# Performance work log

Measured on AMD Instinct MI355X. Metric: run time of the kernel, lower is better.

The kernel has to match this reference:

```python
import jax, jax.numpy as jnp
import numpy as np

B, S, D = 64, 4096, 1024

def setup_inputs() -> dict:
    key = jax.random.key(0)
    k1, k2, k3, k4, k5, k6 = jax.random.split(key, 6)
    scale = 1.0 / np.sqrt(D)
    return {
        "query": jax.random.normal(k1, (B, D), dtype=jnp.float32),
        "context": jax.random.normal(k2, (B, S, D), dtype=jnp.float32),
        "context_mask": jax.random.randint(k3, (B, S), 0, 2, dtype=jnp.int32),
        "W_align": jax.random.normal(k4, (D, D), dtype=jnp.float32) * scale,
        "W_context": jax.random.normal(k5, (D, D), dtype=jnp.float32) * scale,
        "W_query": jax.random.normal(k6, (D, D), dtype=jnp.float32) * scale,
    }

def reference(query, context, context_mask, W_align, W_context, W_query):
    # alignment_function == 'general': q = query @ W_align.T   [B, D]
    q = query @ W_align.T
    # scores: context [B,S,D] bmm q [B,D,1] -> [B,S]
    align = jnp.einsum('bsd,bd->bs', context, q)
    align = jnp.where(context_mask == 0, -jnp.inf, align)
    attention = jax.nn.softmax(align, axis=-1)              # [B, S]
    weight_context = jnp.einsum('bs,bsd->bd', attention, context)  # [B, D]
    out = jnp.tanh(weight_context @ W_context.T + query @ W_query.T)
    return out, attention, weight_context
```

## Files before the change

kernel.cpp:

```cpp
#include <hip/hip_runtime.h>
#include <cstddef>
#include <cstdint>

#define B_ 64
#define S_ 4096
#define D_ 1024
#define CHUNKS 16
#define ROWS (S_ / CHUNKS)

__global__ __launch_bounds__(256) void small_gemm(
    const float* __restrict__ A1, const float* __restrict__ W1,
    const float* __restrict__ A2, const float* __restrict__ W2,
    float* __restrict__ C, int do_tanh)
{
    int t = threadIdx.x;
    int i = blockIdx.x * 4 + (t & 3);
    int b = t >> 2;

    const float4* A14 = (const float4*)(A1 + (size_t)b * D_);
    const float4* W14 = (const float4*)(W1 + (size_t)i * D_);
    float acc = 0.f;
#pragma unroll 4
    for (int k = 0; k < D_ / 4; ++k) {
        float4 a = A14[k];
        float4 w = W14[k];
        acc += a.x * w.x + a.y * w.y + a.z * w.z + a.w * w.w;
    }
    if (A2 != nullptr) {
        const float4* A24 = (const float4*)(A2 + (size_t)b * D_);
        const float4* W24 = (const float4*)(W2 + (size_t)i * D_);
#pragma unroll 4
        for (int k = 0; k < D_ / 4; ++k) {
            float4 a = A24[k];
            float4 w = W24[k];
            acc += a.x * w.x + a.y * w.y + a.z * w.z + a.w * w.w;
        }
    }
    if (do_tanh) acc = tanhf(acc);
    C[(size_t)b * D_ + i] = acc;
}

__global__ __launch_bounds__(256) void pass1(
    const float* __restrict__ ctx,
    const int* __restrict__ mask,
    const float* __restrict__ q,
    float* __restrict__ align_out,
    float* __restrict__ pm,
    float* __restrict__ pl,
    float* __restrict__ pacc)
{
    int b = blockIdx.y, c = blockIdx.x, t = threadIdx.x;
    int wave = t >> 6, lane = t & 63;

    __shared__ float4 qs[256];
    __shared__ float red[2][4][4];

    qs[t] = ((const float4*)(q + (size_t)b * D_))[t];
    __syncthreads();
    float4 qv = qs[t];

    const float* cb = ctx + (size_t)b * S_ * D_ + (size_t)c * ROWS * D_;
    const int* mb = mask + (size_t)b * S_ + c * ROWS;
    float* ab = align_out + (size_t)b * S_ + c * ROWS;

    float m = -1e30f, l = 0.f;
    float a0 = 0.f, a1 = 0.f, a2 = 0.f, a3 = 0.f;

    for (int r0 = 0; r0 < ROWS; r0 += 4) {
        int buf = (r0 >> 2) & 1;
        float4 v0 = ((const float4*)(cb + (size_t)(r0 + 0) * D_))[t];
        float4 v1 = ((const float4*)(cb + (size_t)(r0 + 1) * D_))[t];
        float4 v2 = ((const float4*)(cb + (size_t)(r0 + 2) * D_))[t];
        float4 v3 = ((const float4*)(cb + (size_t)(r0 + 3) * D_))[t];

        float p0 = v0.x * qv.x + v0.y * qv.y + v0.z * qv.z + v0.w * qv.w;
        float p1 = v1.x * qv.x + v1.y * qv.y + v1.z * qv.z + v1.w * qv.w;
        float p2 = v2.x * qv.x + v2.y * qv.y + v2.z * qv.z + v2.w * qv.w;
        float p3 = v3.x * qv.x + v3.y * qv.y + v3.z * qv.z + v3.w * qv.w;

#pragma unroll
        for (int off = 32; off > 0; off >>= 1) {
            p0 += __shfl_down(p0, off);
            p1 += __shfl_down(p1, off);
            p2 += __shfl_down(p2, off);
            p3 += __shfl_down(p3, off);
        }
        if (lane == 0) {
            red[buf][wave][0] = p0;
            red[buf][wave][1] = p1;
            red[buf][wave][2] = p2;
            red[buf][wave][3] = p3;
        }
        __syncthreads();

        float s0 = red[buf][0][0] + red[buf][1][0] + red[buf][2][0] + red[buf][3][0];
        float s1 = red[buf][0][1] + red[buf][1][1] + red[buf][2][1] + red[buf][3][1];
        float s2 = red[buf][0][2] + red[buf][1][2] + red[buf][2][2] + red[buf][3][2];
        float s3 = red[buf][0][3] + red[buf][1][3] + red[buf][2][3] + red[buf][3][3];

        int m0 = mb[r0 + 0], m1 = mb[r0 + 1], m2 = mb[r0 + 2], m3 = mb[r0 + 3];
        s0 = m0 ? s0 : -1e30f;
        s1 = m1 ? s1 : -1e30f;
        s2 = m2 ? s2 : -1e30f;
        s3 = m3 ? s3 : -1e30f;

        if (t == 0) {
            ab[r0 + 0] = s0;
            ab[r0 + 1] = s1;
            ab[r0 + 2] = s2;
            ab[r0 + 3] = s3;
        }

        float nm = fmaxf(m, fmaxf(fmaxf(s0, s1), fmaxf(s2, s3)));
        float alpha = expf(m - nm);
        float e0 = (s0 <= -1e29f) ? 0.f : expf(s0 - nm);
        float e1 = (s1 <= -1e29f) ? 0.f : expf(s1 - nm);
        float e2 = (s2 <= -1e29f) ? 0.f : expf(s2 - nm);
        float e3 = (s3 <= -1e29f) ? 0.f : expf(s3 - nm);

        l = l * alpha + (e0 + e1 + e2 + e3);
        a0 = a0 * alpha + e0 * v0.x + e1 * v1.x + e2 * v2.x + e3 * v3.x;
        a1 = a1 * alpha + e0 * v0.y + e1 * v1.y + e2 * v2.y + e3 * v3.y;
        a2 = a2 * alpha + e0 * v0.z + e1 * v1.z + e2 * v2.z + e3 * v3.z;
        a3 = a3 * alpha + e0 * v0.w + e1 * v1.w + e2 * v2.w + e3 * v3.w;
        m = nm;
    }

    int idx = b * CHUNKS + c;
    if (t == 0) {
        pm[idx] = m;
        pl[idx] = l;
    }
    float4 av;
    av.x = a0; av.y = a1; av.z = a2; av.w = a3;
    ((float4*)(pacc + (size_t)idx * D_))[t] = av;
}

__global__ __launch_bounds__(256) void combine(
    const float* __restrict__ pm, const float* __restrict__ pl,
    const float* __restrict__ pacc,
    float* __restrict__ wc, float* __restrict__ ml)
{
    int b = blockIdx.x, t = threadIdx.x;
    float m = -1e30f;
#pragma unroll
    for (int c = 0; c < CHUNKS; ++c) m = fmaxf(m, pm[b * CHUNKS + c]);
    float l = 0.f;
    float w[CHUNKS];
#pragma unroll
    for (int c = 0; c < CHUNKS; ++c) {
        w[c] = expf(pm[b * CHUNKS + c] - m);
        l += pl[b * CHUNKS + c] * w[c];
    }
    float inv = (l > 0.f) ? 1.f / l : 0.f;
    float ax = 0.f, ay = 0.f, az = 0.f, aw = 0.f;
#pragma unroll
    for (int c = 0; c < CHUNKS; ++c) {
        float4 a = ((const float4*)(pacc + (size_t)(b * CHUNKS + c) * D_))[t];
        ax += a.x * w[c];
        ay += a.y * w[c];
        az += a.z * w[c];
        aw += a.w * w[c];
    }
    float4 r;
    r.x = ax * inv; r.y = ay * inv; r.z = az * inv; r.w = aw * inv;
    ((float4*)(wc + (size_t)b * D_))[t] = r;
    if (t == 0) {
        ml[b * 2 + 0] = m;
        ml[b * 2 + 1] = l;
    }
}

__global__ __launch_bounds__(256) void finalize_att(
    float* __restrict__ att, const float* __restrict__ ml)
{
    int idx = blockIdx.x * 256 + threadIdx.x;
    int b = idx >> 12;
    float s = att[idx];
    float m = ml[b * 2 + 0], l = ml[b * 2 + 1];
    float v = (s <= -1e29f || !(l > 0.f)) ? 0.f : expf(s - m) / l;
    att[idx] = v;
}

extern "C" void kernel_launch(void* const* d_in, const int* in_sizes, int n_in,
                              void* d_out, int out_size, void* d_ws, size_t ws_size,
                              hipStream_t stream)
{
    const float* query     = (const float*)d_in[0];
    const float* ctx       = (const float*)d_in[1];
    const int*   mask      = (const int*)d_in[2];
    const float* W_align   = (const float*)d_in[3];
    const float* W_context = (const float*)d_in[4];
    const float* W_query   = (const float*)d_in[5];

    float* out = (float*)d_out;
    float* att = out + B_ * D_;
    float* wc  = att + B_ * S_;

    float* ws    = (float*)d_ws;
    float* qproj = ws;
    float* pm    = qproj + B_ * D_;
    float* pl    = pm + B_ * CHUNKS;
    float* ml    = pl + B_ * CHUNKS;
    float* pacc  = ml + 2 * B_;

    small_gemm<<<dim3(D_ / 4), 256, 0, stream>>>(query, W_align, nullptr, nullptr, qproj, 0);

    pass1<<<dim3(CHUNKS, B_), 256, 0, stream>>>(ctx, mask, qproj, att, pm, pl, pacc);

    combine<<<dim3(B_), 256, 0, stream>>>(pm, pl, pacc, wc, ml);

    finalize_att<<<dim3(B_ * S_ / 256), 256, 0, stream>>>(att, ml);

    small_gemm<<<dim3(D_ / 4), 256, 0, stream>>>(wc, W_context, query, W_query, out, 1);
}
```

Measured before the change: 1.461 ms.

## Give each wave its own row chunk to drop block-level syncs in pass1

pass1 now assigns every wave an independent run of context rows. Each lane holds a full 1024-wide row slice as four float4 loads, so row dot products finish with a wave-level xor shuffle instead of shared-memory reduction and a __syncthreads per four rows. This quadruples the number of partial softmax chunks, so combine reads and merges 64 partials per batch instead of 16. small_gemm also gets four independent accumulators for more ILP. Register pressure in pass1 rises sharply, with 16 float4 loads plus 16 accumulators per lane, which may lower occupancy.

```diff
diff --git a/kernel.cpp b/kernel.cpp
--- a/kernel.cpp
+++ b/kernel.cpp
@@ -5,8 +5,14 @@
 #define B_ 64
 #define S_ 4096
 #define D_ 1024
-#define CHUNKS 16
-#define ROWS (S_ / CHUNKS)
+#define NBLK 16
+#define WAVES 4
+#define NCH (NBLK * WAVES)
+#define WROWS (S_ / NCH)
+
+__device__ __forceinline__ float dot4(float4 a, float4 b) {
+    return a.x * b.x + a.y * b.y + a.z * b.z + a.w * b.w;
+}
 
 __global__ __launch_bounds__(256) void small_gemm(
     const float* __restrict__ A1, const float* __restrict__ W1,
@@ -19,23 +25,34 @@
 
     const float4* A14 = (const float4*)(A1 + (size_t)b * D_);
     const float4* W14 = (const float4*)(W1 + (size_t)i * D_);
-    float acc = 0.f;
-#pragma unroll 4
-    for (int k = 0; k < D_ / 4; ++k) {
-        float4 a = A14[k];
-        float4 w = W14[k];
-        acc += a.x * w.x + a.y * w.y + a.z * w.z + a.w * w.w;
+    float acc0 = 0.f, acc1 = 0.f, acc2 = 0.f, acc3 = 0.f;
+#pragma unroll 2
+    for (int k = 0; k < D_ / 4; k += 4) {
+        float4 a0 = A14[k + 0], w0 = W14[k + 0];
+        float4 a1 = A14[k + 1], w1 = W14[k + 1];
+        float4 a2 = A14[k + 2], w2 = W14[k + 2];
+        float4 a3 = A14[k + 3], w3 = W14[k + 3];
+        acc0 += dot4(a0, w0);
+        acc1 += dot4(a1, w1);
+        acc2 += dot4(a2, w2);
+        acc3 += dot4(a3, w3);
     }
     if (A2 != nullptr) {
         const float4* A24 = (const float4*)(A2 + (size_t)b * D_);
         const float4* W24 = (const float4*)(W2 + (size_t)i * D_);
-#pragma unroll 4
-        for (int k = 0; k < D_ / 4; ++k) {
-            float4 a = A24[k];
-            float4 w = W24[k];
-            acc += a.x * w.x + a.y * w.y + a.z * w.z + a.w * w.w;
+#pragma unroll 2
+        for (int k = 0; k < D_ / 4; k += 4) {
+            float4 a0 = A24[k + 0], w0 = W24[k + 0];
+            float4 a1 = A24[k + 1], w1 = W24[k + 1];
+            float4 a2 = A24[k + 2], w2 = W24[k + 2];
+            float4 a3 = A24[k + 3], w3 = W24[k + 3];
+            acc0 += dot4(a0, w0);
+            acc1 += dot4(a1, w1);
+            acc2 += dot4(a2, w2);
+            acc3 += dot4(a3, w3);
         }
     }
+    float acc = (acc0 + acc1) + (acc2 + acc3);
     if (do_tanh) acc = tanhf(acc);
     C[(size_t)b * D_ + i] = acc;
 }
@@ -49,67 +66,57 @@
     float* __restrict__ pl,
     float* __restrict__ pacc)
 {
-    int b = blockIdx.y, c = blockIdx.x, t = threadIdx.x;
-    int wave = t >> 6, lane = t & 63;
-
-    __shared__ float4 qs[256];
-    __shared__ float red[2][4][4];
-
-    qs[t] = ((const float4*)(q + (size_t)b * D_))[t];
-    __syncthreads();
-    float4 qv = qs[t];
-
-    const float* cb = ctx + (size_t)b * S_ * D_ + (size_t)c * ROWS * D_;
-    const int* mb = mask + (size_t)b * S_ + c * ROWS;
-    float* ab = align_out + (size_t)b * S_ + c * ROWS;
+    int b = blockIdx.y;
+    int lane = threadIdx.x & 63;
+    int c = blockIdx.x * WAVES + (threadIdx.x >> 6);
+
+    const float4* qb = (const float4*)(q + (size_t)b * D_);
+    float4 q0 = qb[lane];
+    float4 q1 = qb[lane + 64];
+    float4 q2 = qb[lane + 128];
+    float4 q3 = qb[lane + 192];
+
+    const float4* cb = (const float4*)(ctx + (size_t)b * S_ * D_ + (size_t)c * WROWS * D_);
+    const int* mb = mask + (size_t)b * S_ + c * WROWS;
+    float* ab = align_out + (size_t)b * S_ + c * WROWS;
 
     float m = -1e30f, l = 0.f;
-    float a0 = 0.f, a1 = 0.f, a2 = 0.f, a3 = 0.f;
-
-    for (int r0 = 0; r0 < ROWS; r0 += 4) {
-        int buf = (r0 >> 2) & 1;
-        float4 v0 = ((const float4*)(cb + (size_t)(r0 + 0) * D_))[t];
-        float4 v1 = ((const float4*)(cb + (size_t)(r0 + 1) * D_))[t];
-        float4 v2 = ((const float4*)(cb + (size_t)(r0 + 2) * D_))[t];
-        float4 v3 = ((const float4*)(cb + (size_t)(r0 + 3) * D_))[t];
-
-        float p0 = v0.x * qv.x + v0.y * qv.y + v0.z * qv.z + v0.w * qv.w;
-        float p1 = v1.x * qv.x + v1.y * qv.y + v1.z * qv.z + v1.w * qv.w;
-        float p2 = v2.x * qv.x + v2.y * qv.y + v2.z * qv.z + v2.w * qv.w;
-        float p3 = v3.x * qv.x + v3.y * qv.y + v3.z * qv.z + v3.w * qv.w;
+    float4 a0 = make_float4(0.f, 0.f, 0.f, 0.f);
+    float4 a1 = a0, a2 = a0, a3 = a0;
+
+    for (int r0 = 0; r0 < WROWS; r0 += 4) {
+        const float4* row0 = cb + (size_t)(r0 + 0) * (D_ / 4);
+        const float4* row1 = cb + (size_t)(r0 + 1) * (D_ / 4);
+        const float4* row2 = cb + (size_t)(r0 + 2) * (D_ / 4);
+        const float4* row3 = cb + (size_t)(r0 + 3) * (D_ / 4);
+
+        float4 v00 = row0[lane], v01 = row0[lane + 64], v02 = row0[lane + 128], v03 = row0[lane + 192];
+        float4 v10 = row1[lane], v11 = row1[lane + 64], v12 = row1[lane + 128], v13 = row1[lane + 192];
+        float4 v20 = row2[lane], v21 = row2[lane + 64], v22 = row2[lane + 128], v23 = row2[lane + 192];
+        float4 v30 = row3[lane], v31 = row3[lane + 64], v32 = row3[lane + 128], v33 = row3[lane + 192];
+
+        int mk0 = mb[r0 + 0], mk1 = mb[r0 + 1], mk2 = mb[r0 + 2], mk3 = mb[r0 + 3];
+
+        float p0 = dot4(v00, q0) + dot4(v01, q1) + dot4(v02, q2) + dot4(v03, q3);
+        float p1 = dot4(v10, q0) + dot4(v11, q1) + dot4(v12, q2) + dot4(v13, q3);
+        float p2 = dot4(v20, q0) + dot4(v21, q1) + dot4(v22, q2) + dot4(v23, q3);
+        float p3 = dot4(v30, q0) + dot4(v31, q1) + dot4(v32, q2) + dot4(v33, q3);
 
 #pragma unroll
         for (int off = 32; off > 0; off >>= 1) {
-            p0 += __shfl_down(p0, off);
-            p1 += __shfl_down(p1, off);
-            p2 += __shfl_down(p2, off);
-            p3 += __shfl_down(p3, off);
+            p0 += __shfl_xor(p0, off);
+            p1 += __shfl_xor(p1, off);
+            p2 += __shfl_xor(p2, off);
+            p3 += __shfl_xor(p3, off);
         }
-        if (lane == 0) {
-            red[buf][wave][0] = p0;
-            red[buf][wave][1] = p1;
-            red[buf][wave][2] = p2;
-            red[buf][wave][3] = p3;
-        }
-        __syncthreads();
-
-        float s0 = red[buf][0][0] + red[buf][1][0] + red[buf][2][0] + red[buf][3][0];
-        float s1 = red[buf][0][1] + red[buf][1][1] + red[buf][2][1] + red[buf][3][1];
-        float s2 = red[buf][0][2] + red[buf][1][2] + red[buf][2][2] + red[buf][3][2];
-        float s3 = red[buf][0][3] + red[buf][1][3] + red[buf][2][3] + red[buf][3][3];
-
-        int m0 = mb[r0 + 0], m1 = mb[r0 + 1], m2 = mb[r0 + 2], m3 = mb[r0 + 3];
-        s0 = m0 ? s0 : -1e30f;
-        s1 = m1 ? s1 : -1e30f;
-        s2 = m2 ? s2 : -1e30f;
-        s3 = m3 ? s3 : -1e30f;
-
-        if (t == 0) {
-            ab[r0 + 0] = s0;
-            ab[r0 + 1] = s1;
-            ab[r0 + 2] = s2;
-            ab[r0 + 3] = s3;
-        }
+
+        float s0 = mk0 ? p0 : -1e30f;
+        float s1 = mk1 ? p1 : -1e30f;
+        float s2 = mk2 ? p2 : -1e30f;
+        float s3 = mk3 ? p3 : -1e30f;
+
+        float sv = (lane == 0) ? s0 : (lane == 1) ? s1 : (lane == 2) ? s2 : s3;
+        if (lane < 4) ab[r0 + lane] = sv;
 
         float nm = fmaxf(m, fmaxf(fmaxf(s0, s1), fmaxf(s2, s3)));
         float alpha = expf(m - nm);
@@ -119,21 +126,40 @@
         float e3 = (s3 <= -1e29f) ? 0.f : expf(s3 - nm);
 
         l = l * alpha + (e0 + e1 + e2 + e3);
-        a0 = a0 * alpha + e0 * v0.x + e1 * v1.x + e2 * v2.x + e3 * v3.x;
-        a1 = a1 * alpha + e0 * v0.y + e1 * v1.y + e2 * v2.y + e3 * v3.y;
-        a2 = a2 * alpha + e0 * v0.z + e1 * v1.z + e2 * v2.z + e3 * v3.z;
-        a3 = a3 * alpha + e0 * v0.w + e1 * v1.w + e2 * v2.w + e3 * v3.w;
+
+        a0.x = a0.x * alpha + e0 * v00.x + e1 * v10.x + e2 * v20.x + e3 * v30.x;
+        a0.y = a0.y * alpha + e0 * v00.y + e1 * v10.y + e2 * v20.y + e3 * v30.y;
+        a0.z = a0.z * alpha + e0 * v00.z + e1 * v10.z + e2 * v20.z + e3 * v30.z;
+        a0.w = a0.w * alpha + e0 * v00.w + e1 * v10.w + e2 * v20.w + e3 * v30.w;
+
+        a1.x = a1.x * alpha + e0 * v01.x + e1 * v11.x + e2 * v21.x + e3 * v31.x;
+        a1.y = a1.y * alpha + e0 * v01.y + e1 * v11.y + e2 * v21.y + e3 * v31.y;
+        a1.z = a1.z * alpha + e0 * v01.z + e1 * v11.z + e2 * v21.z + e3 * v31.z;
+        a1.w = a1.w * alpha + e0 * v01.w + e1 * v11.w + e2 * v21.w + e3 * v31.w;
+
+        a2.x = a2.x * alpha + e0 * v02.x + e1 * v12.x + e2 * v22.x + e3 * v32.x;
+        a2.y = a2.y * alpha + e0 * v02.y + e1 * v12.y + e2 * v22.y + e3 * v32.y;
+        a2.z = a2.z * alpha + e0 * v02.z + e1 * v12.z + e2 * v22.z + e3 * v32.z;
+        a2.w = a2.w * alpha + e0 * v02.w + e1 * v12.w + e2 * v22.w + e3 * v32.w;
+
+        a3.x = a3.x * alpha + e0 * v03.x + e1 * v13.x + e2 * v23.x + e3 * v33.x;
+        a3.y = a3.y * alpha + e0 * v03.y + e1 * v13.y + e2 * v23.y + e3 * v33.y;
+        a3.z = a3.z * alpha + e0 * v03.z + e1 * v13.z + e2 * v23.z + e3 * v33.z;
+        a3.w = a3.w * alpha + e0 * v03.w + e1 * v13.w + e2 * v23.w + e3 * v33.w;
+
         m = nm;
     }
 
-    int idx = b * CHUNKS + c;
-    if (t == 0) {
+    int idx = b * NCH + c;
+    if (lane == 0) {
         pm[idx] = m;
         pl[idx] = l;
     }
-    float4 av;
-    av.x = a0; av.y = a1; av.z = a2; av.w = a3;
-    ((float4*)(pacc + (size_t)idx * D_))[t] = av;
+    float4* pa = (float4*)(pacc + (size_t)idx * D_);
+    pa[lane] = a0;
+    pa[lane + 64] = a1;
+    pa[lane + 128] = a2;
+    pa[lane + 192] = a3;
 }
 
 __global__ __launch_bounds__(256) void combine(
@@ -142,26 +168,27 @@
     float* __restrict__ wc, float* __restrict__ ml)
 {
     int b = blockIdx.x, t = threadIdx.x;
+    const float* pmb = pm + (size_t)b * NCH;
+    const float* plb = pl + (size_t)b * NCH;
+
     float m = -1e30f;
 #pragma unroll
-    for (int c = 0; c < CHUNKS; ++c) m = fmaxf(m, pm[b * CHUNKS + c]);
+    for (int c = 0; c < NCH; ++c) m = fmaxf(m, pmb[c]);
+
     float l = 0.f;
-    float w[CHUNKS];
-#pragma unroll
-    for (int c = 0; c < CHUNKS; ++c) {
-        w[c] = expf(pm[b * CHUNKS + c] - m);
-        l += pl[b * CHUNKS + c] * w[c];
+    float ax = 0.f, ay = 0.f, az = 0.f, aw = 0.f;
+    const float4* pb = (const float4*)(pacc + (size_t)b * NCH * D_);
+#pragma unroll 4
+    for (int c = 0; c < NCH; ++c) {
+        float w = expf(pmb[c] - m);
+        l += plb[c] * w;
+        float4 a = pb[(size_t)c * (D_ / 4) + t];
+        ax += a.x * w;
+        ay += a.y * w;
+        az += a.z * w;
+        aw += a.w * w;
     }
     float inv = (l > 0.f) ? 1.f / l : 0.f;
-    float ax = 0.f, ay = 0.f, az = 0.f, aw = 0.f;
-#pragma unroll
-    for (int c = 0; c < CHUNKS; ++c) {
-        float4 a = ((const float4*)(pacc + (size_t)(b * CHUNKS + c) * D_))[t];
-        ax += a.x * w[c];
-        ay += a.y * w[c];
-        az += a.z * w[c];
-        aw += a.w * w[c];
-    }
     float4 r;
     r.x = ax * inv; r.y = ay * inv; r.z = az * inv; r.w = aw * inv;
     ((float4*)(wc + (size_t)b * D_))[t] = r;
@@ -200,13 +227,13 @@
     float* ws    = (float*)d_ws;
     float* qproj = ws;
     float* pm    = qproj + B_ * D_;
-    float* pl    = pm + B_ * CHUNKS;
-    float* ml    = pl + B_ * CHUNKS;
+    float* pl    = pm + B_ * NCH;
+    float* ml    = pl + B_ * NCH;
     float* pacc  = ml + 2 * B_;
 
     small_gemm<<<dim3(D_ / 4), 256, 0, stream>>>(query, W_align, nullptr, nullptr, qproj, 0);
 
-    pass1<<<dim3(CHUNKS, B_), 256, 0, stream>>>(ctx, mask, qproj, att, pm, pl, pacc);
+    pass1<<<dim3(NBLK, B_), 256, 0, stream>>>(ctx, mask, qproj, att, pm, pl, pacc);
 
     combine<<<dim3(B_), 256, 0, stream>>>(pm, pl, pacc, wc, ml);
 
```

Result: slower. 1.517 ms (+3.9%).
